# Kernel optimization log

Measured on AMD Instinct MI355X. Metric: run time of the kernel, lower is better.

The kernel has to match this reference:

```python
import jax, jax.numpy as jnp
import numpy as np

B, N, C = 16, 2048, 3           # images, proposals/image, classes (incl. background)
K = 100                         # num_detections kept per class
SCORE_THRESH = 0.05
NMS_THRESH = 0.5
MIN_ANGLE = 10.0                # process_box min width (self.min_angle)
WX, WW = 1.0, 1.0               # box_coder reg_weights
NEG = jnp.float32(-1e9)


def setup_inputs() -> dict:
    key = jax.random.key(0)
    k1, k2, k3, k4 = jax.random.split(key, 4)
    class_logit = jax.random.normal(k1, (B, N, C), jnp.float32)
    box_regression = jax.random.normal(k2, (B, N, 2 * C), jnp.float32) * 0.1
    starts = jax.random.uniform(k3, (B, N), dtype=jnp.float32) * 300.0
    widths = jax.random.uniform(k4, (B, N), dtype=jnp.float32) * 50.0 + 12.0
    proposal = jnp.stack([starts, starts + widths], axis=-1)  # [B,N,2] 1-D intervals
    return {"class_logit": class_logit, "box_regression": box_regression,
            "proposal": proposal, "image_shape": 360}


def _decode(delta, prop):
    w = prop[:, 1] - prop[:, 0]
    ctr = prop[:, 0] + 0.5 * w
    dx = delta[:, 0] / WX
    dw = jnp.minimum(delta[:, 1] / WW, 4.0)  # clamp like torchvision
    pc = dx * w + ctr
    pw = jnp.exp(dw) * w
    return jnp.stack([pc - 0.5 * pw, pc + 0.5 * pw], axis=-1)  # [N,2]


def _iou_1d(a, b):
    inter = jnp.maximum(0.0, jnp.minimum(a[:, None, 1], b[None, :, 1])
                        - jnp.maximum(a[:, None, 0], b[None, :, 0]))
    union = (a[:, None, 1] - a[:, None, 0]) + (b[None, :, 1] - b[None, :, 0]) - inter
    return inter / jnp.maximum(union, 1e-8)  # [Na,Nb]


def _infer_one_class(score, delta, prop, image_shape):
    # score [N], delta [N,2], prop [N,2] -> [K,3] (start, end, score); invalid slots score=NEG
    box = _decode(delta, prop)
    lo = jnp.clip(box[:, 0], 0.0, image_shape)
    hi = jnp.clip(box[:, 1], 0.0, image_shape)
    box = jnp.stack([lo, hi], axis=-1)
    valid = ((hi - lo) >= MIN_ANGLE) & (score >= SCORE_THRESH)
    ms = jnp.where(valid, score, NEG)
    order = jnp.argsort(-ms)
    b = box[order]
    s = ms[order]
    sup = jax.lax.stop_gradient(_iou_1d(b, b)) > NMS_THRESH  # [N,N] bool
    idx = jnp.arange(N)

    def body(keep, i):  # greedy NMS in score order
        kill = sup[i] & keep[i] & (idx > i)
        return keep & ~kill, None

    keep0 = s > 0.5 * NEG
    keep, _ = jax.lax.scan(body, keep0, idx)
    ks = jnp.where(keep, s, NEG)
    top_s, top_i = jax.lax.top_k(ks, K)
    top_b = b[top_i]
    return jnp.concatenate([top_b, top_s[:, None]], axis=-1)  # [K,3]


def reference(class_logit, box_regression, proposal, image_shape):
    img = jnp.float32(image_shape)
    scores = jax.nn.softmax(class_logit, axis=-1)[..., 1:]        # [B,N,C-1] fg classes
    deltas = box_regression.reshape(B, N, C, 2)[:, :, 1:]         # [B,N,C-1,2]
    scores = jnp.moveaxis(scores, -1, 1)                          # [B,C-1,N]
    deltas = jnp.moveaxis(deltas, 2, 1)                           # [B,C-1,N,2]
    f = jax.vmap(jax.vmap(_infer_one_class, in_axes=(0, 0, None, None)),
                 in_axes=(0, 0, 0, None))
    return f(scores, deltas, proposal, img)  # [B, C-1, K, 3]
```

## Files before the change

kernel.cpp:

```cpp
#include <hip/hip_runtime.h>
#include <math.h>

#define B_IMG 16
#define N_PROP 2048
#define C_CLS 3
#define K_OUT 100
#define NTHREADS 1024
#define NWAVES (NTHREADS / 64)
#define NBLK64 (N_PROP / 64)
#define NUNITS (B_IMG * N_PROP)

__device__ __forceinline__ unsigned long long shfl_xor_u64(unsigned long long v, int lx) {
    unsigned int lo = (unsigned int)__shfl_xor((int)(unsigned int)(v & 0xffffffffull), lx, 64);
    unsigned int hi = (unsigned int)__shfl_xor((int)(unsigned int)(v >> 32), lx, 64);
    return ((unsigned long long)hi << 32) | (unsigned long long)lo;
}
__device__ __forceinline__ float readlane_f(float v, int l) {
    return __int_as_float(__builtin_amdgcn_readlane(__float_as_int(v), l));
}
__device__ __forceinline__ unsigned long long readlane_u64(unsigned long long v, int l) {
    unsigned int lo = (unsigned int)__builtin_amdgcn_readlane((int)(unsigned int)(v & 0xffffffffull), l);
    unsigned int hi = (unsigned int)__builtin_amdgcn_readlane((int)(unsigned int)(v >> 32), l);
    return ((unsigned long long)hi << 32) | (unsigned long long)lo;
}
__device__ __forceinline__ bool iou_gt_half(float inter, float uni) {
    double b = (double)fmaxf(uni, 1e-8f);
    return (double)inter * 2.0 > b * 0x1.000001p0;
}
__device__ __forceinline__ float parse_imgf(int raw) {
    return (raw > 0 && raw < 1000000) ? (float)raw : __int_as_float(raw);
}

__global__ __launch_bounds__(256)
void decode_kernel(const float* __restrict__ class_logit,
                   const float* __restrict__ box_reg,
                   const float* __restrict__ proposal,
                   const int* __restrict__ image_shape_p,
                   unsigned long long* __restrict__ wskey,
                   float2* __restrict__ wbox)
{
#pragma clang fp contract(off)
    const int t = blockIdx.x * 256 + threadIdx.x;
    const int n = t & (N_PROP - 1);
    const float imgf = parse_imgf(image_shape_p[0]);

    const float* lg = class_logit + (size_t)t * C_CLS;
    float l0 = lg[0], l1 = lg[1], l2 = lg[2];
    float mx = fmaxf(l0, fmaxf(l1, l2));
    float e0 = (float)exp((double)(l0 - mx));
    float e1 = (float)exp((double)(l1 - mx));
    float e2 = (float)exp((double)(l2 - mx));
    float denom = (e0 + e1) + e2;

    const float* pp = proposal + (size_t)t * 2;
    float pA = pp[0], pB = pp[1];
    float w = pB - pA;
    float ctr = pA + 0.5f * w;

    const float* dr = box_reg + (size_t)t * (2 * C_CLS);
    float d1x = dr[2], d1w = dr[3], d2x = dr[4], d2w = dr[5];

#pragma unroll
    for (int c = 0; c < 2; ++c) {
        float score = ((c == 0) ? e1 : e2) / denom;
        float dx = (c == 0) ? d1x : d2x;
        float dw = fminf((c == 0) ? d1w : d2w, 4.0f);
        float tt = dx * w;
        float pc = tt + ctr;
        float pw = (float)exp((double)dw) * w;
        float half = 0.5f * pw;
        float lo = pc - half;
        float hi = pc + half;
        lo = fminf(fmaxf(lo, 0.0f), imgf);
        hi = fminf(fmaxf(hi, 0.0f), imgf);
        bool valid = ((hi - lo) >= 10.0f) && (score >= 0.05f);
        float ms = valid ? score : -1e9f;
        unsigned int u = __float_as_uint(ms);
        unsigned int e = (u & 0x80000000u) ? ~u : (u | 0x80000000u);
        wskey[c * NUNITS + t] = ((unsigned long long)e << 32) |
                                (unsigned long long)(0xFFFFFFFFu - (unsigned int)n);
        wbox[c * NUNITS + t] = make_float2(lo, hi);
    }
}

__global__ __launch_bounds__(NTHREADS)
void roiheads_kernel(const unsigned long long* __restrict__ wskey,
                     const float2* __restrict__ wbox,
                     float* __restrict__ out)
{
#pragma clang fp contract(off)
    __shared__ unsigned long long skey[N_PROP];
    __shared__ float slo[N_PROP], shi[N_PROP];
    __shared__ unsigned char keep[N_PROP];
    __shared__ unsigned short alv[2][N_PROP];
    __shared__ float clo[64], chi[64];
    __shared__ unsigned long long sup[64];
    __shared__ unsigned long long kmask[NBLK64];
    __shared__ int wsum[NWAVES];
    __shared__ int sh_nvalid;

    const int tid = threadIdx.x;
    const int lane = tid & 63;
    const int wid = tid >> 6;
    const int img = blockIdx.x >> 1;
    const int cls = blockIdx.x & 1;
    const size_t base = (size_t)cls * NUNITS + (size_t)img * N_PROP;

    if (tid == 0) sh_nvalid = 0;

    const int p0 = (wid << 7) | (lane << 1);
    const int p1 = p0 | 1;

    unsigned long long r0 = wskey[base + p0];
    unsigned long long r1 = wskey[base + p1];

    auto pass_inreg = [&](int k, int j) {
        if (j == 1) {
            bool desc = ((p0 & k) == 0);
            bool sw = desc ? (r0 < r1) : (r0 > r1);
            if (sw) { unsigned long long t = r0; r0 = r1; r1 = t; }
        } else {
            int lx = j >> 1;
            unsigned long long o0 = shfl_xor_u64(r0, lx);
            unsigned long long o1 = shfl_xor_u64(r1, lx);
            bool desc = ((p0 & k) == 0);
            bool lower = ((p0 & j) == 0);
            bool takeMax = (lower == desc);
            r0 = takeMax ? (r0 > o0 ? r0 : o0) : (r0 < o0 ? r0 : o0);
            r1 = takeMax ? (r1 > o1 ? r1 : o1) : (r1 < o1 ? r1 : o1);
        }
    };

    for (int k = 2; k <= 128; k <<= 1)
        for (int j = k >> 1; j >= 1; j >>= 1)
            pass_inreg(k, j);

    for (int k = 256; k <= N_PROP; k <<= 1) {
        skey[p0] = r0; skey[p1] = r1;
        __syncthreads();
        for (int j = k >> 1; j >= 128; j >>= 1) {
            int i = ((tid & ~(j - 1)) << 1) | (tid & (j - 1));
            int part = i | j;
            unsigned long long a = skey[i], b = skey[part];
            bool desc_blk = ((i & k) == 0);
            bool sw = desc_blk ? (a < b) : (a > b);
            if (sw) { skey[i] = b; skey[part] = a; }
            __syncthreads();
        }
        r0 = skey[p0]; r1 = skey[p1];
        for (int j = 64; j >= 1; j >>= 1)
            pass_inreg(k, j);
    }
    skey[p0] = r0; skey[p1] = r1;
    __syncthreads();

    for (int i = tid; i < N_PROP; i += NTHREADS) {
        unsigned long long kk = skey[i];
        unsigned int e = (unsigned int)(kk >> 32);
        unsigned int sb = (e & 0x80000000u) ? (e & 0x7FFFFFFFu) : ~e;
        float s = __uint_as_float(sb);
        unsigned int n = 0xFFFFFFFFu - (unsigned int)(kk & 0xFFFFFFFFull);
        float2 bx = wbox[base + n];
        slo[i] = bx.x;
        shi[i] = bx.y;
        keep[i] = 0;
        bool v = (s > -5e8f);
        unsigned long long mb = __ballot(v);
        if (lane == 0) atomicAdd(&sh_nvalid, __popcll(mb));
        alv[0][i] = (unsigned short)i;
    }
    __syncthreads();

    int na = sh_nvalid;
    int cur = 0;
    int tk = 0;
    const unsigned long long below = (1ull << lane) - 1ull;

    while (na > 0) {
        const int m = (na < 64) ? na : 64;

        unsigned short cp = alv[cur][lane];
        bool cin = (lane < m);
        float qloc = cin ? slo[cp] : 0.0f;
        float qhic = cin ? shi[cp] : 0.0f;

#pragma unroll
        for (int rr4 = 0; rr4 < 4; ++rr4) {
            int rr = (wid << 2) | rr4;
            unsigned long long row = 0;
            if (rr < m) {
                unsigned short rp = alv[cur][rr];
                float rlo = slo[rp], rhi = shi[rp];
                float inter = fmaxf(fminf(rhi, qhic) - fmaxf(rlo, qloc), 0.0f);
                float uni = (rhi - rlo) + (qhic - qloc) - inter;
                bool kill = cin && (lane > rr) && iou_gt_half(inter, uni);
                row = __ballot(kill);
            }
            if (lane == 0) sup[rr] = row;
        }
        __syncthreads();

        unsigned long long rw = sup[lane];
        unsigned long long A = (m >= 64) ? ~0ull : ((1ull << m) - 1ull);
        unsigned long long kept = 0;
        while (A) {
            int c = __builtin_ctzll(A);
            kept |= (1ull << c);
            A &= ~(readlane_u64(rw, c) | (1ull << c));
        }
        const int cnt = __popcll(kept);

        if (wid == 0) {
            bool alive = cin && ((kept >> lane) & 1ull);
            if (alive) {
                keep[cp] = 1;
                int rank = __popcll(kept & below);
                clo[rank] = qloc; chi[rank] = qhic;
            }
        }
        __syncthreads();
        tk += cnt;
        if (tk >= K_OUT) break;

        float klo = 0.0f, khi = 0.0f;
        if (lane < cnt) { klo = clo[lane]; khi = chi[lane]; }
        int base2 = 0;
        for (int start = 64; start < na; start += NTHREADS) {
            int t2 = start + tid;
            unsigned short q = 0;
            bool surv = false;
            if (t2 < na) {
                q = alv[cur][t2];
                float qlo = slo[q], qhi = shi[q];
                float qw = qhi - qlo;
                bool dead = false;
                for (int r = 0; r < cnt; ++r) {
                    float cl = readlane_f(klo, r);
                    float ch = readlane_f(khi, r);
                    float inter = fmaxf(fminf(qhi, ch) - fmaxf(qlo, cl), 0.0f);
                    float uni = qw + (ch - cl) - inter;
                    dead |= iou_gt_half(inter, uni);
                }
                surv = !dead;
            }
            unsigned long long mb = __ballot(surv);
            if (lane == 0) wsum[wid] = __popcll(mb);
            __syncthreads();
            int off = base2, tot = base2;
            for (int w2 = 0; w2 < NWAVES; ++w2) {
                int c2 = wsum[w2];
                if (w2 < wid) off += c2;
                tot += c2;
            }
            if (surv) alv[cur ^ 1][off + __popcll(mb & below)] = q;
            base2 = tot;
            __syncthreads();
        }
        na = base2;
        cur ^= 1;
    }

    for (int blk = wid; blk < NBLK64; blk += NWAVES) {
        bool kk = keep[blk * 64 + lane] != 0;
        unsigned long long mb = __ballot(kk);
        if (lane == 0) kmask[blk] = mb;
    }
    __syncthreads();
    {
        float* outp = out + (((size_t)img * 2 + cls) * K_OUT) * 3;
        for (int blk = wid; blk < NBLK64; blk += NWAVES) {
            int kc = 0, nc = 0, nk = 0;
            for (int b = 0; b < NBLK64; ++b) {
                int pc = __popcll(kmask[b]);
                nk += pc;
                if (b < blk) { kc += pc; nc += 64 - pc; }
            }
            if (kc >= K_OUT && nk + nc >= K_OUT && nc >= K_OUT) continue;
            int p = blk * 64 + lane;
            unsigned long long mb = kmask[blk];
            bool k = (mb >> lane) & 1ull;
            int rk = kc + __popcll(mb & below);
            int rn = nc + __popcll((~mb) & below);
            if (k) {
                if (rk < K_OUT) {
                    unsigned long long kk2 = skey[p];
                    unsigned int e = (unsigned int)(kk2 >> 32);
                    unsigned int sb = (e & 0x80000000u) ? (e & 0x7FFFFFFFu) : ~e;
                    outp[rk * 3 + 0] = slo[p];
                    outp[rk * 3 + 1] = shi[p];
                    outp[rk * 3 + 2] = __uint_as_float(sb);
                }
            } else {
                int oi = nk + rn;
                if (oi < K_OUT) {
                    outp[oi * 3 + 0] = slo[p];
                    outp[oi * 3 + 1] = shi[p];
                    outp[oi * 3 + 2] = -1e9f;
                }
            }
        }
    }
}

extern "C" void kernel_launch(void* const* d_in, const int* in_sizes, int n_in,
                              void* d_out, int out_size, void* d_ws, size_t ws_size,
                              hipStream_t stream) {
    const float* class_logit = (const float*)d_in[0];
    const float* box_reg     = (const float*)d_in[1];
    const float* prop        = (const float*)d_in[2];
    const int*   image_shape = (const int*)d_in[3];
    float* out = (float*)d_out;

    unsigned long long* wskey = (unsigned long long*)d_ws;
    float2* wbox = (float2*)((char*)d_ws + 2 * NUNITS * sizeof(unsigned long long));

    decode_kernel<<<dim3(NUNITS / 256), dim3(256), 0, stream>>>(
        class_logit, box_reg, prop, image_shape, wskey, wbox);
    roiheads_kernel<<<dim3(B_IMG * 2), dim3(NTHREADS), 0, stream>>>(
        wskey, wbox, out);
}
```

Baseline: 97.94 us.

## Move early bitonic sort stages into decode kernel across more blocks

The decode kernel now also sorts 512-key runs per (image, class), alternating ascending and descending runs so they form bitonic sequences. It is launched as 128 blocks. The roiheads kernel then starts its bitonic sort at stage k=1024, skipping the earlier stages that ran on only 32 blocks. This spreads sort work over more CUs and reduces serial work in the low-occupancy NMS kernel, at the cost of a heavier decode kernel with fewer threads per element and extra shared-memory syncs.

```diff
diff --git a/kernel.cpp b/kernel.cpp
--- a/kernel.cpp
+++ b/kernel.cpp
@@ -9,6 +9,8 @@
 #define NWAVES (NTHREADS / 64)
 #define NBLK64 (N_PROP / 64)
 #define NUNITS (B_IMG * N_PROP)
+#define NTHA 256
+#define RUN 512
 
 __device__ __forceinline__ unsigned long long shfl_xor_u64(unsigned long long v, int lx) {
     unsigned int lo = (unsigned int)__shfl_xor((int)(unsigned int)(v & 0xffffffffull), lx, 64);
@@ -31,40 +33,48 @@
     return (raw > 0 && raw < 1000000) ? (float)raw : __int_as_float(raw);
 }
 
-__global__ __launch_bounds__(256)
-void decode_kernel(const float* __restrict__ class_logit,
-                   const float* __restrict__ box_reg,
-                   const float* __restrict__ proposal,
-                   const int* __restrict__ image_shape_p,
-                   unsigned long long* __restrict__ wskey,
-                   float2* __restrict__ wbox)
+__global__ __launch_bounds__(NTHA)
+void decode_sort_kernel(const float* __restrict__ class_logit,
+                        const float* __restrict__ box_reg,
+                        const float* __restrict__ proposal,
+                        const int* __restrict__ image_shape_p,
+                        unsigned long long* __restrict__ wskey,
+                        float2* __restrict__ wbox)
 {
 #pragma clang fp contract(off)
-    const int t = blockIdx.x * 256 + threadIdx.x;
-    const int n = t & (N_PROP - 1);
+    __shared__ unsigned long long skey[RUN];
+
+    const int tid = threadIdx.x;
+    const int lane = tid & 63;
+    const int wid = tid >> 6;
+    const int u = blockIdx.x >> 2;
+    const int q = blockIdx.x & 3;
+    const int img = u >> 1;
+    const int cls = u & 1;
+    const bool flip = (q & 1) != 0;
+    const int off = q * RUN;
+    const size_t base = (size_t)cls * NUNITS + (size_t)img * N_PROP;
     const float imgf = parse_imgf(image_shape_p[0]);
 
-    const float* lg = class_logit + (size_t)t * C_CLS;
-    float l0 = lg[0], l1 = lg[1], l2 = lg[2];
-    float mx = fmaxf(l0, fmaxf(l1, l2));
-    float e0 = (float)exp((double)(l0 - mx));
-    float e1 = (float)exp((double)(l1 - mx));
-    float e2 = (float)exp((double)(l2 - mx));
-    float denom = (e0 + e1) + e2;
-
-    const float* pp = proposal + (size_t)t * 2;
-    float pA = pp[0], pB = pp[1];
-    float w = pB - pA;
-    float ctr = pA + 0.5f * w;
-
-    const float* dr = box_reg + (size_t)t * (2 * C_CLS);
-    float d1x = dr[2], d1w = dr[3], d2x = dr[4], d2w = dr[5];
-
-#pragma unroll
-    for (int c = 0; c < 2; ++c) {
-        float score = ((c == 0) ? e1 : e2) / denom;
-        float dx = (c == 0) ? d1x : d2x;
-        float dw = fminf((c == 0) ? d1w : d2w, 4.0f);
+    for (int i = tid; i < RUN; i += NTHA) {
+        const int n = off + i;
+        const size_t g = (size_t)img * N_PROP + n;
+        const float* lg = class_logit + g * C_CLS;
+        float l0 = lg[0], l1 = lg[1], l2 = lg[2];
+        float mx = fmaxf(l0, fmaxf(l1, l2));
+        float e0 = (float)exp((double)(l0 - mx));
+        float e1 = (float)exp((double)(l1 - mx));
+        float e2 = (float)exp((double)(l2 - mx));
+        float denom = (e0 + e1) + e2;
+        float score = ((cls == 0) ? e1 : e2) / denom;
+
+        const float* dr = box_reg + g * (2 * C_CLS) + 2 * (cls + 1);
+        float dx = dr[0];
+        float dw = fminf(dr[1], 4.0f);
+        const float* pp = proposal + g * 2;
+        float pA = pp[0], pB = pp[1];
+        float w = pB - pA;
+        float ctr = pA + 0.5f * w;
         float tt = dx * w;
         float pc = tt + ctr;
         float pw = (float)exp((double)dw) * w;
@@ -75,12 +85,56 @@
         hi = fminf(fmaxf(hi, 0.0f), imgf);
         bool valid = ((hi - lo) >= 10.0f) && (score >= 0.05f);
         float ms = valid ? score : -1e9f;
-        unsigned int u = __float_as_uint(ms);
-        unsigned int e = (u & 0x80000000u) ? ~u : (u | 0x80000000u);
-        wskey[c * NUNITS + t] = ((unsigned long long)e << 32) |
-                                (unsigned long long)(0xFFFFFFFFu - (unsigned int)n);
-        wbox[c * NUNITS + t] = make_float2(lo, hi);
-    }
+        wbox[base + n] = make_float2(lo, hi);
+        unsigned int uu = __float_as_uint(ms);
+        unsigned int e = (uu & 0x80000000u) ? ~uu : (uu | 0x80000000u);
+        skey[i] = ((unsigned long long)e << 32) |
+                  (unsigned long long)(0xFFFFFFFFu - (unsigned int)n);
+    }
+    __syncthreads();
+
+    const int p0 = (wid << 7) | (lane << 1);
+    const int p1 = p0 | 1;
+    unsigned long long r0 = skey[p0], r1 = skey[p1];
+
+    auto pass_inreg = [&](int k, int j) {
+        bool desc = (((p0 & k) == 0) != flip);
+        if (j == 1) {
+            bool sw = desc ? (r0 < r1) : (r0 > r1);
+            if (sw) { unsigned long long t = r0; r0 = r1; r1 = t; }
+        } else {
+            int lx = j >> 1;
+            unsigned long long o0 = shfl_xor_u64(r0, lx);
+            unsigned long long o1 = shfl_xor_u64(r1, lx);
+            bool lower = ((p0 & j) == 0);
+            bool takeMax = (lower == desc);
+            r0 = takeMax ? (r0 > o0 ? r0 : o0) : (r0 < o0 ? r0 : o0);
+            r1 = takeMax ? (r1 > o1 ? r1 : o1) : (r1 < o1 ? r1 : o1);
+        }
+    };
+
+    for (int k = 2; k <= 128; k <<= 1)
+        for (int j = k >> 1; j >= 1; j >>= 1)
+            pass_inreg(k, j);
+
+    for (int k = 256; k <= RUN; k <<= 1) {
+        skey[p0] = r0; skey[p1] = r1;
+        __syncthreads();
+        for (int j = k >> 1; j >= 128; j >>= 1) {
+            int i = ((tid & ~(j - 1)) << 1) | (tid & (j - 1));
+            int part = i | j;
+            unsigned long long a = skey[i], b = skey[part];
+            bool desc_blk = (((i & k) == 0) != flip);
+            bool sw = desc_blk ? (a < b) : (a > b);
+            if (sw) { skey[i] = b; skey[part] = a; }
+            __syncthreads();
+        }
+        r0 = skey[p0]; r1 = skey[p1];
+        for (int j = 64; j >= 1; j >>= 1)
+            pass_inreg(k, j);
+    }
+    wskey[base + off + p0] = r0;
+    wskey[base + off + p1] = r1;
 }
 
 __global__ __launch_bounds__(NTHREADS)
@@ -131,11 +185,7 @@
         }
     };
 
-    for (int k = 2; k <= 128; k <<= 1)
-        for (int j = k >> 1; j >= 1; j >>= 1)
-            pass_inreg(k, j);
-
-    for (int k = 256; k <= N_PROP; k <<= 1) {
+    for (int k = 1024; k <= N_PROP; k <<= 1) {
         skey[p0] = r0; skey[p1] = r1;
         __syncthreads();
         for (int j = k >> 1; j >= 128; j >>= 1) {
@@ -227,11 +277,11 @@
         int base2 = 0;
         for (int start = 64; start < na; start += NTHREADS) {
             int t2 = start + tid;
-            unsigned short q = 0;
+            unsigned short qq = 0;
             bool surv = false;
             if (t2 < na) {
-                q = alv[cur][t2];
-                float qlo = slo[q], qhi = shi[q];
+                qq = alv[cur][t2];
+                float qlo = slo[qq], qhi = shi[qq];
                 float qw = qhi - qlo;
                 bool dead = false;
                 for (int r = 0; r < cnt; ++r) {
@@ -246,13 +296,13 @@
             unsigned long long mb = __ballot(surv);
             if (lane == 0) wsum[wid] = __popcll(mb);
             __syncthreads();
-            int off = base2, tot = base2;
+            int off2 = base2, tot = base2;
             for (int w2 = 0; w2 < NWAVES; ++w2) {
                 int c2 = wsum[w2];
-                if (w2 < wid) off += c2;
+                if (w2 < wid) off2 += c2;
                 tot += c2;
             }
-            if (surv) alv[cur ^ 1][off + __popcll(mb & below)] = q;
+            if (surv) alv[cur ^ 1][off2 + __popcll(mb & below)] = qq;
             base2 = tot;
             __syncthreads();
         }
@@ -314,7 +364,7 @@
     unsigned long long* wskey = (unsigned long long*)d_ws;
     float2* wbox = (float2*)((char*)d_ws + 2 * NUNITS * sizeof(unsigned long long));
 
-    decode_kernel<<<dim3(NUNITS / 256), dim3(256), 0, stream>>>(
+    decode_sort_kernel<<<dim3(B_IMG * 2 * 4), dim3(NTHA), 0, stream>>>(
         class_logit, box_reg, prop, image_shape, wskey, wbox);
     roiheads_kernel<<<dim3(B_IMG * 2), dim3(NTHREADS), 0, stream>>>(
         wskey, wbox, out);
```

New measurement: 95.12 us. 1.03x faster.
